# Performance work log

Hardware: AMD Instinct MI355X
Metric: run time of the kernel (lower is better)

Reference implementation:

```python
import jax, jax.numpy as jnp
import numpy as np


def _sparse_mask(T, S, W, G):
    """Replicates CustomSparseAttention._create_sparse_mask (bool [T, S])."""
    ii = np.arange(T)[:, None]
    jj = np.arange(S)[None, :]
    # local sliding window: cols in [i - W//2, i + W//2]
    m = (jj >= ii - W // 2) & (jj <= ii + W // 2)
    # overlapping block windows every (W - W//4) rows
    ov = W // 4
    for i in range(0, T, W - ov):
        m[i:i + W, max(0, i - ov):min(S, i + W + ov)] = True
    # strided global tokens
    if G > 0:
        stride = S // (G + 1)
        gi = np.linspace(stride, S - stride, G).astype(np.int64)  # torch .long() truncates
        m[:, gi] = True
    # diagonal +/- 1
    m |= np.abs(jj - ii) <= 1
    return jnp.asarray(m)


def setup_inputs() -> dict:
    key = jax.random.key(0)
    ks = jax.random.split(key, 8)
    B, T, S, E = 2, 2048, 2048, 512
    std = 0.02
    return {
        "query": jax.random.normal(ks[0], (B, T, E), jnp.float32),
        "key": jax.random.normal(ks[1], (B, S, E), jnp.float32),
        "value": jax.random.normal(ks[2], (B, S, E), jnp.float32),
        "Wq": jax.random.normal(ks[3], (E, E), jnp.float32) * std,
        "bq": jnp.zeros((E,), jnp.float32),
        "Wk": jax.random.normal(ks[4], (E, E), jnp.float32) * std,
        "bk": jnp.zeros((E,), jnp.float32),
        "Wv": jax.random.normal(ks[5], (E, E), jnp.float32) * std,
        "bv": jnp.zeros((E,), jnp.float32),
        "Wo": jax.random.normal(ks[6], (E, E), jnp.float32) * std,
        "bo": jnp.zeros((E,), jnp.float32),
        "temperature": jnp.ones((1,), jnp.float32) * 0.1,
        "local_window_size": 128,
        "num_global_tokens": 16,
    }


def reference(query, key, value, Wq, bq, Wk, bk, Wv, bv, Wo, bo,
              temperature, local_window_size, num_global_tokens):
    B, T, E = query.shape
    S = key.shape[1]
    H = 16
    hd = E // H
    scaling = float(hd) ** -0.5

    q = (query @ Wq.T + bq) * scaling          # [B, T, E]
    k = key @ Wk.T + bk                        # [B, S, E]
    v = value @ Wv.T + bv                      # [B, S, E]

    q = q.reshape(B, T, H, hd)
    k = k.reshape(B, S, H, hd)
    v = v.reshape(B, S, H, hd)

    # [B, H, T, S] dense scores, scaled by learned temperature
    attn = jnp.einsum('bthd,bshd->bhts', q, k) * temperature[0]

    mask = _sparse_mask(T, S, local_window_size, num_global_tokens)  # [T, S] bool
    attn = jnp.where(mask[None, None], attn, -jnp.inf)

    # (row-max subtraction in the original is the standard stable softmax)
    attn = jax.nn.softmax(attn, axis=-1)

    out = jnp.einsum('bhts,bshd->bthd', attn, v).reshape(B, T, E)
    out = out @ Wo.T + bo
    return out
```

## Files before the change

### kernel.cpp

```cpp
#include <hip/hip_runtime.h>

typedef _Float16 f16x8 __attribute__((ext_vector_type(8)));
typedef float f32x4 __attribute__((ext_vector_type(4)));

#define Tt 2048
#define Ee 512
#define Hh 16
#define HD 32
#define Bb 2
#define Mm (Bb*Tt)

__device__ __constant__ int GCOLS[16] = {120,240,361,481,602,722,843,963,
                                         1084,1204,1325,1445,1566,1686,1807,1928};

__device__ __forceinline__ int lo_of(int i) {
    int kmin = (i >= 32) ? ((i - 32) / 96) : 0;
    int lo = kmin * 96 - 32;
    return lo < 0 ? 0 : lo;
}
__device__ __forceinline__ int hi_of(int i) {
    int hi = (i / 96) * 96 + 160;
    return hi > Tt ? Tt : hi;
}

__device__ __forceinline__ f16x8 cvt8(float4 a, float4 b) {
    f16x8 r;
    r[0]=(_Float16)a.x; r[1]=(_Float16)a.y; r[2]=(_Float16)a.z; r[3]=(_Float16)a.w;
    r[4]=(_Float16)b.x; r[5]=(_Float16)b.y; r[6]=(_Float16)b.z; r[7]=(_Float16)b.w;
    return r;
}

__device__ __forceinline__ void async_copy16(const _Float16* g, _Float16* l) {
    __builtin_amdgcn_global_load_lds(
        (const __attribute__((address_space(1))) void*)g,
        (__attribute__((address_space(3))) void*)l, 16, 0, 0);
}

__global__ __launch_bounds__(256)
void cvt_kernel(const float* __restrict__ q, const float* __restrict__ k,
                const float* __restrict__ v,
                const float* __restrict__ wq, const float* __restrict__ wk,
                const float* __restrict__ wv, const float* __restrict__ wo,
                _Float16* __restrict__ dst)
{
    const int g8 = blockIdx.x * 256 + threadIdx.x;
    const float* src;
    if (g8 < 786432) {
        const int s = g8 >> 18;
        const float* xs = (s == 0) ? q : (s == 1) ? k : v;
        src = xs + (size_t)(g8 & 262143) * 8;
    } else {
        const int w8 = g8 - 786432;
        const int s = w8 >> 15;
        const float* ws = (s == 0) ? wq : (s == 1) ? wk : (s == 2) ? wv : wo;
        src = ws + (size_t)(w8 & 32767) * 8;
    }
    float4 a = ((const float4*)src)[0];
    float4 b = ((const float4*)src)[1];
    *(f16x8*)(dst + (size_t)g8 * 8) = cvt8(a, b);
}

__global__ __launch_bounds__(256)
void proj_kernel(const _Float16* __restrict__ xw,
                 const float* __restrict__ bq, const float* __restrict__ bk,
                 const float* __restrict__ bv, const float* __restrict__ temp,
                 _Float16* __restrict__ q_ws, _Float16* __restrict__ k_ws,
                 _Float16* __restrict__ v_ws)
{
    const int z = blockIdx.z;
    const _Float16* A = xw + (size_t)z * (Mm * Ee);
    const _Float16* W = xw + (size_t)3 * Mm * Ee + (size_t)z * (Ee * Ee);
    const float* bias = (z == 0) ? bq : (z == 1) ? bk : bv;

    const int m0 = blockIdx.x * 64;
    const int n0 = blockIdx.y * 128;

    __shared__ _Float16 Ash[64 * 64];
    __shared__ _Float16 Bsh[128 * 64];

    const int tid  = threadIdx.x;
    const int lane = tid & 63, wave = tid >> 6;
    const int quad = lane >> 4, l16 = lane & 15;
    const int wm = wave & 1, wn = wave >> 1;

    const int sl = lane >> 3;
    const int lcol = ((lane & 7) ^ sl) * 8;
    const _Float16* aSrc0 = A + (size_t)(m0 + wave*8       + sl) * Ee + lcol;
    const _Float16* aSrc1 = A + (size_t)(m0 + (4+wave)*8   + sl) * Ee + lcol;
    const _Float16* bSrc0 = W + (size_t)(n0 + wave*8       + sl) * Ee + lcol;
    const _Float16* bSrc1 = W + (size_t)(n0 + (4+wave)*8   + sl) * Ee + lcol;
    const _Float16* bSrc2 = W + (size_t)(n0 + (8+wave)*8   + sl) * Ee + lcol;
    const _Float16* bSrc3 = W + (size_t)(n0 + (12+wave)*8  + sl) * Ee + lcol;
    _Float16* aDst0 = Ash + wave*512;
    _Float16* aDst1 = Ash + (4+wave)*512;
    _Float16* bDst0 = Bsh + wave*512;
    _Float16* bDst1 = Bsh + (4+wave)*512;
    _Float16* bDst2 = Bsh + (8+wave)*512;
    _Float16* bDst3 = Bsh + (12+wave)*512;

    f32x4 acc[2][4] = {};

    for (int k0 = 0; k0 < Ee; k0 += 64) {
        __syncthreads();
        async_copy16(aSrc0 + k0, aDst0);
        async_copy16(aSrc1 + k0, aDst1);
        async_copy16(bSrc0 + k0, bDst0);
        async_copy16(bSrc1 + k0, bDst1);
        async_copy16(bSrc2 + k0, bDst2);
        async_copy16(bSrc3 + k0, bDst3);
        __syncthreads();

        #pragma unroll
        for (int kk = 0; kk < 2; kk++) {
            f16x8 af[2], bf[4];
            #pragma unroll
            for (int mt = 0; mt < 2; mt++) {
                const int row = wm*32 + mt*16 + l16;
                af[mt] = *(const f16x8*)&Ash[row*64 + (((kk*4+quad) ^ (row & 7)) * 8)];
            }
            #pragma unroll
            for (int nt = 0; nt < 4; nt++) {
                const int row = wn*64 + nt*16 + l16;
                bf[nt] = *(const f16x8*)&Bsh[row*64 + (((kk*4+quad) ^ (row & 7)) * 8)];
            }
            #pragma unroll
            for (int mt = 0; mt < 2; mt++)
                #pragma unroll
                for (int nt = 0; nt < 4; nt++)
                    acc[mt][nt] = __builtin_amdgcn_mfma_f32_16x16x32_f16(af[mt], bf[nt], acc[mt][nt], 0, 0, 0);
        }
    }

    const float scale = (z == 0) ? (0.17677669529663687f * temp[0]) : 1.0f;
    #pragma unroll
    for (int nt = 0; nt < 4; nt++) {
        const int n = n0 + wn * 64 + nt * 16 + l16;
        const float bn = bias[n];
        const int h = n >> 5, d = n & 31;
        #pragma unroll
        for (int mt = 0; mt < 2; mt++) {
            #pragma unroll
            for (int r = 0; r < 4; r++) {
                const int m = m0 + wm * 32 + mt * 16 + quad * 4 + r;
                const float val = (acc[mt][nt][r] + bn) * scale;
                const int bidx = m >> 11, t = m & (Tt - 1);
                if (z == 2) {
                    v_ws[((size_t)(bidx * Hh + h) * HD + d) * Tt + t] = (_Float16)val;
                } else {
                    _Float16* dst = (z == 0) ? q_ws : k_ws;
                    dst[((size_t)(bidx * Hh + h) * Tt + t) * HD + d] = (_Float16)val;
                }
            }
        }
    }
}

__global__ __launch_bounds__(256)
void attn_kernel(const _Float16* __restrict__ q_ws, const _Float16* __restrict__ k_ws,
                 const _Float16* __restrict__ v_ws, _Float16* __restrict__ o_ws)
{
    const int qb = blockIdx.x * 64;
    const int h  = blockIdx.y;
    const int b  = blockIdx.z;
    const int bh = b * Hh + h;

    const int tid  = threadIdx.x;
    const int lane = tid & 63, wave = tid >> 6;
    const int quad = lane >> 4, l16 = lane & 15;
    const int t0   = qb + wave * 16;

    __shared__ _Float16 P_lds[4][16*72];
    _Float16* myP = &P_lds[wave][0];

    const f16x8 qf = *(const f16x8*)(q_ws + ((size_t)bh*Tt + t0 + l16)*HD + quad*8);

    int lo[4], len[4];
    #pragma unroll
    for (int r = 0; r < 4; r++) {
        const int i = t0 + quad*4 + r;
        lo[r] = lo_of(i); len[r] = hi_of(i) - lo[r];
    }

    float lsum[4] = {0.f, 0.f, 0.f, 0.f};
    f32x4 accO[2] = {};
    const f32x4 zf = {0.f, 0.f, 0.f, 0.f};

    {
        const int gj = GCOLS[l16];
        const f16x8 kg = *(const f16x8*)(k_ws + ((size_t)bh*Tt + gj)*HD + quad*8);
        const f32x4 s = __builtin_amdgcn_mfma_f32_16x16x32_f16(qf, kg, zf, 0, 0, 0);
        #pragma unroll
        for (int r = 0; r < 4; r++) {
            const bool inside = (unsigned)(gj - lo[r]) < (unsigned)len[r];
            const float p = inside ? 0.f : __expf(s[r]);
            const _Float16 ph = (_Float16)p;
            lsum[r] += (float)ph;
            myP[(quad*4 + r)*72 + l16] = ph;
        }
        f16x8 pf;
        if (quad < 2) pf = *(const f16x8*)&myP[l16*72 + quad*8];
        else {
            #pragma unroll
            for (int j = 0; j < 8; j++) pf[j] = (_Float16)0.f;
        }
        int gck[8];
        #pragma unroll
        for (int j = 0; j < 8; j++) gck[j] = (quad < 2) ? GCOLS[quad*8 + j] : 0;
        #pragma unroll
        for (int dt = 0; dt < 2; dt++) {
            f16x8 vg;
            if (quad < 2) {
                const _Float16* vrow = v_ws + ((size_t)bh*HD + dt*16 + l16)*Tt;
                #pragma unroll
                for (int j = 0; j < 8; j++) vg[j] = vrow[gck[j]];
            } else {
                #pragma unroll
                for (int j = 0; j < 8; j++) vg[j] = (_Float16)0.f;
            }
            accO[dt] = __builtin_amdgcn_mfma_f32_16x16x32_f16(pf, vg, accO[dt], 0, 0, 0);
        }
    }

    const int cstart = lo_of(t0) & ~63;
    const int cend   = hi_of(t0 + 15);
    for (int j0 = cstart; j0 < cend; j0 += 64) {
        f16x8 kf[4]; f32x4 s[4];
        #pragma unroll
        for (int nt = 0; nt < 4; nt++)
            kf[nt] = *(const f16x8*)(k_ws + ((size_t)bh*Tt + j0 + nt*16 + l16)*HD + quad*8);
        #pragma unroll
        for (int nt = 0; nt < 4; nt++)
            s[nt] = __builtin_amdgcn_mfma_f32_16x16x32_f16(qf, kf[nt], zf, 0, 0, 0);
        #pragma unroll
        for (int nt = 0; nt < 4; nt++) {
            const int j = j0 + nt*16 + l16;
            #pragma unroll
            for (int r = 0; r < 4; r++) {
                const bool inside = (unsigned)(j - lo[r]) < (unsigned)len[r];
                const float p = inside ? __expf(s[nt][r]) : 0.f;
                const _Float16 ph = (_Float16)p;
                lsum[r] += (float)ph;
                myP[(quad*4 + r)*72 + nt*16 + l16] = ph;
            }
        }
        #pragma unroll
        for (int kt = 0; kt < 2; kt++) {
            const f16x8 pf = *(const f16x8*)&myP[l16*72 + kt*32 + quad*8];
            #pragma unroll
            for (int dt = 0; dt < 2; dt++) {
                const f16x8 vf = *(const f16x8*)(v_ws + ((size_t)bh*HD + dt*16 + l16)*Tt
                                                 + j0 + kt*32 + quad*8);
                accO[dt] = __builtin_amdgcn_mfma_f32_16x16x32_f16(pf, vf, accO[dt], 0, 0, 0);
            }
        }
    }

    #pragma unroll
    for (int r = 0; r < 4; r++) {
        float v = lsum[r];
        v += __shfl_xor(v, 1);
        v += __shfl_xor(v, 2);
        v += __shfl_xor(v, 4);
        v += __shfl_xor(v, 8);
        lsum[r] = 1.0f / v;
    }
    #pragma unroll
    for (int dt = 0; dt < 2; dt++) {
        #pragma unroll
        for (int r = 0; r < 4; r++) {
            const int t = t0 + quad*4 + r;
            const int d = dt*16 + l16;
            o_ws[((size_t)(b*Tt + t)*Hh + h)*HD + d] = (_Float16)(accO[dt][r] * lsum[r]);
        }
    }
}

__global__ __launch_bounds__(256)
void out_kernel(const _Float16* __restrict__ Aw, const _Float16* __restrict__ Wof,
                const float* __restrict__ bo, float* __restrict__ out)
{
    const int m0 = blockIdx.x * 64;
    const int n0 = blockIdx.y * 128;

    __shared__ _Float16 Ash[64 * 64];
    __shared__ _Float16 Bsh[128 * 64];

    const int tid  = threadIdx.x;
    const int lane = tid & 63, wave = tid >> 6;
    const int quad = lane >> 4, l16 = lane & 15;
    const int wm = wave & 1, wn = wave >> 1;

    const int sl = lane >> 3;
    const int lcol = ((lane & 7) ^ sl) * 8;
    const _Float16* aSrc0 = Aw  + (size_t)(m0 + wave*8      + sl) * Ee + lcol;
    const _Float16* aSrc1 = Aw  + (size_t)(m0 + (4+wave)*8  + sl) * Ee + lcol;
    const _Float16* bSrc0 = Wof + (size_t)(n0 + wave*8      + sl) * Ee + lcol;
    const _Float16* bSrc1 = Wof + (size_t)(n0 + (4+wave)*8  + sl) * Ee + lcol;
    const _Float16* bSrc2 = Wof + (size_t)(n0 + (8+wave)*8  + sl) * Ee + lcol;
    const _Float16* bSrc3 = Wof + (size_t)(n0 + (12+wave)*8 + sl) * Ee + lcol;
    _Float16* aDst0 = Ash + wave*512;
    _Float16* aDst1 = Ash + (4+wave)*512;
    _Float16* bDst0 = Bsh + wave*512;
    _Float16* bDst1 = Bsh + (4+wave)*512;
    _Float16* bDst2 = Bsh + (8+wave)*512;
    _Float16* bDst3 = Bsh + (12+wave)*512;

    f32x4 acc[2][4] = {};

    for (int k0 = 0; k0 < Ee; k0 += 64) {
        __syncthreads();
        async_copy16(aSrc0 + k0, aDst0);
        async_copy16(aSrc1 + k0, aDst1);
        async_copy16(bSrc0 + k0, bDst0);
        async_copy16(bSrc1 + k0, bDst1);
        async_copy16(bSrc2 + k0, bDst2);
        async_copy16(bSrc3 + k0, bDst3);
        __syncthreads();

        #pragma unroll
        for (int kk = 0; kk < 2; kk++) {
            f16x8 af[2], bf[4];
            #pragma unroll
            for (int mt = 0; mt < 2; mt++) {
                const int row = wm*32 + mt*16 + l16;
                af[mt] = *(const f16x8*)&Ash[row*64 + (((kk*4+quad) ^ (row & 7)) * 8)];
            }
            #pragma unroll
            for (int nt = 0; nt < 4; nt++) {
                const int row = wn*64 + nt*16 + l16;
                bf[nt] = *(const f16x8*)&Bsh[row*64 + (((kk*4+quad) ^ (row & 7)) * 8)];
            }
            #pragma unroll
            for (int mt = 0; mt < 2; mt++)
                #pragma unroll
                for (int nt = 0; nt < 4; nt++)
                    acc[mt][nt] = __builtin_amdgcn_mfma_f32_16x16x32_f16(af[mt], bf[nt], acc[mt][nt], 0, 0, 0);
        }
    }

    #pragma unroll
    for (int nt = 0; nt < 4; nt++) {
        const int n = n0 + wn * 64 + nt * 16 + l16;
        const float bn = bo[n];
        #pragma unroll
        for (int mt = 0; mt < 2; mt++) {
            #pragma unroll
            for (int r = 0; r < 4; r++) {
                const int m = m0 + wm * 32 + mt * 16 + quad * 4 + r;
                out[(size_t)m * Ee + n] = acc[mt][nt][r] + bn;
            }
        }
    }
}

extern "C" void kernel_launch(void* const* d_in, const int* in_sizes, int n_in,
                              void* d_out, int out_size, void* d_ws, size_t ws_size,
                              hipStream_t stream)
{
    const float* query = (const float*)d_in[0];
    const float* key_  = (const float*)d_in[1];
    const float* value = (const float*)d_in[2];
    const float* Wq    = (const float*)d_in[3];
    const float* bq    = (const float*)d_in[4];
    const float* Wk    = (const float*)d_in[5];
    const float* bk    = (const float*)d_in[6];
    const float* Wv    = (const float*)d_in[7];
    const float* bv    = (const float*)d_in[8];
    const float* Wo    = (const float*)d_in[9];
    const float* bo    = (const float*)d_in[10];
    const float* temp  = (const float*)d_in[11];

    _Float16* xw   = (_Float16*)d_ws;
    _Float16* q_ws = xw + 7340032;
    _Float16* k_ws = q_ws + (size_t)Mm * Ee;
    _Float16* v_ws = k_ws + (size_t)Mm * Ee;
    _Float16* o_ws = v_ws + (size_t)Mm * Ee;
    const _Float16* Wof = xw + (size_t)3 * Mm * Ee + (size_t)3 * Ee * Ee;
    float* out = (float*)d_out;

    cvt_kernel<<<3584, 256, 0, stream>>>(query, key_, value, Wq, Wk, Wv, Wo, xw);
    proj_kernel<<<dim3(64, 4, 3), 256, 0, stream>>>(xw, bq, bk, bv, temp,
                                                    q_ws, k_ws, v_ws);
    attn_kernel<<<dim3(32, 16, 2), 256, 0, stream>>>(q_ws, k_ws, v_ws, o_ws);
    out_kernel<<<dim3(64, 4), 256, 0, stream>>>(o_ws, Wof, bo, out);
}
```

Baseline: 142.1 us.

## Double-buffer LDS tiles in projection and output GEMM kernels

```diff
diff --git a/kernel.cpp b/kernel.cpp
--- a/kernel.cpp
+++ b/kernel.cpp
@@ -75,8 +75,8 @@
     const int m0 = blockIdx.x * 64;
     const int n0 = blockIdx.y * 128;
 
-    __shared__ _Float16 Ash[64 * 64];
-    __shared__ _Float16 Bsh[128 * 64];
+    __shared__ _Float16 Ash[2][64 * 64];
+    __shared__ _Float16 Bsh[2][128 * 64];
 
     const int tid  = threadIdx.x;
     const int lane = tid & 63, wave = tid >> 6;
@@ -91,24 +91,31 @@
     const _Float16* bSrc1 = W + (size_t)(n0 + (4+wave)*8   + sl) * Ee + lcol;
     const _Float16* bSrc2 = W + (size_t)(n0 + (8+wave)*8   + sl) * Ee + lcol;
     const _Float16* bSrc3 = W + (size_t)(n0 + (12+wave)*8  + sl) * Ee + lcol;
-    _Float16* aDst0 = Ash + wave*512;
-    _Float16* aDst1 = Ash + (4+wave)*512;
-    _Float16* bDst0 = Bsh + wave*512;
-    _Float16* bDst1 = Bsh + (4+wave)*512;
-    _Float16* bDst2 = Bsh + (8+wave)*512;
-    _Float16* bDst3 = Bsh + (12+wave)*512;
+
+#define PROJ_STAGE(BUF, K0)                                          \
+    do {                                                             \
+        async_copy16(aSrc0 + (K0), &Ash[BUF][ wave    * 512]);       \
+        async_copy16(aSrc1 + (K0), &Ash[BUF][( 4+wave)* 512]);       \
+        async_copy16(bSrc0 + (K0), &Bsh[BUF][ wave    * 512]);       \
+        async_copy16(bSrc1 + (K0), &Bsh[BUF][( 4+wave)* 512]);       \
+        async_copy16(bSrc2 + (K0), &Bsh[BUF][( 8+wave)* 512]);       \
+        async_copy16(bSrc3 + (K0), &Bsh[BUF][(12+wave)* 512]);       \
+    } while (0)
 
     f32x4 acc[2][4] = {};
 
-    for (int k0 = 0; k0 < Ee; k0 += 64) {
-        __syncthreads();
-        async_copy16(aSrc0 + k0, aDst0);
-        async_copy16(aSrc1 + k0, aDst1);
-        async_copy16(bSrc0 + k0, bDst0);
-        async_copy16(bSrc1 + k0, bDst1);
-        async_copy16(bSrc2 + k0, bDst2);
-        async_copy16(bSrc3 + k0, bDst3);
-        __syncthreads();
+    PROJ_STAGE(0, 0);
+
+    #pragma unroll
+    for (int it = 0; it < 8; ++it) {
+        const int cur = it & 1;
+        if (it < 7) {
+            PROJ_STAGE(cur ^ 1, (it + 1) * 64);
+            asm volatile("s_waitcnt vmcnt(6)" ::: "memory");
+        } else {
+            asm volatile("s_waitcnt vmcnt(0)" ::: "memory");
+        }
+        __builtin_amdgcn_s_barrier();
 
         #pragma unroll
         for (int kk = 0; kk < 2; kk++) {
@@ -116,12 +123,12 @@
             #pragma unroll
             for (int mt = 0; mt < 2; mt++) {
                 const int row = wm*32 + mt*16 + l16;
-                af[mt] = *(const f16x8*)&Ash[row*64 + (((kk*4+quad) ^ (row & 7)) * 8)];
+                af[mt] = *(const f16x8*)&Ash[cur][row*64 + (((kk*4+quad) ^ (row & 7)) * 8)];
             }
             #pragma unroll
             for (int nt = 0; nt < 4; nt++) {
                 const int row = wn*64 + nt*16 + l16;
-                bf[nt] = *(const f16x8*)&Bsh[row*64 + (((kk*4+quad) ^ (row & 7)) * 8)];
+                bf[nt] = *(const f16x8*)&Bsh[cur][row*64 + (((kk*4+quad) ^ (row & 7)) * 8)];
             }
             #pragma unroll
             for (int mt = 0; mt < 2; mt++)
@@ -129,7 +136,9 @@
                 for (int nt = 0; nt < 4; nt++)
                     acc[mt][nt] = __builtin_amdgcn_mfma_f32_16x16x32_f16(af[mt], bf[nt], acc[mt][nt], 0, 0, 0);
         }
-    }
+        __builtin_amdgcn_s_barrier();
+    }
+#undef PROJ_STAGE
 
     const float scale = (z == 0) ? (0.17677669529663687f * temp[0]) : 1.0f;
     #pragma unroll
@@ -282,8 +291,8 @@
     const int m0 = blockIdx.x * 64;
     const int n0 = blockIdx.y * 128;
 
-    __shared__ _Float16 Ash[64 * 64];
-    __shared__ _Float16 Bsh[128 * 64];
+    __shared__ _Float16 Ash[2][64 * 64];
+    __shared__ _Float16 Bsh[2][128 * 64];
 
     const int tid  = threadIdx.x;
     const int lane = tid & 63, wave = tid >> 6;
@@ -298,24 +307,31 @@
     const _Float16* bSrc1 = Wof + (size_t)(n0 + (4+wave)*8  + sl) * Ee + lcol;
     const _Float16* bSrc2 = Wof + (size_t)(n0 + (8+wave)*8  + sl) * Ee + lcol;
     const _Float16* bSrc3 = Wof + (size_t)(n0 + (12+wave)*8 + sl) * Ee + lcol;
-    _Float16* aDst0 = Ash + wave*512;
-    _Float16* aDst1 = Ash + (4+wave)*512;
-    _Float16* bDst0 = Bsh + wave*512;
-    _Float16* bDst1 = Bsh + (4+wave)*512;
-    _Float16* bDst2 = Bsh + (8+wave)*512;
-    _Float16* bDst3 = Bsh + (12+wave)*512;
+
+#define OUT_STAGE(BUF, K0)                                           \
+    do {                                                             \
+        async_copy16(aSrc0 + (K0), &Ash[BUF][ wave    * 512]);       \
+        async_copy16(aSrc1 + (K0), &Ash[BUF][( 4+wave)* 512]);       \
+        async_copy16(bSrc0 + (K0), &Bsh[BUF][ wave    * 512]);       \
+        async_copy16(bSrc1 + (K0), &Bsh[BUF][( 4+wave)* 512]);       \
+        async_copy16(bSrc2 + (K0), &Bsh[BUF][( 8+wave)* 512]);       \
+        async_copy16(bSrc3 + (K0), &Bsh[BUF][(12+wave)* 512]);       \
+    } while (0)
 
     f32x4 acc[2][4] = {};
 
-    for (int k0 = 0; k0 < Ee; k0 += 64) {
-        __syncthreads();
-        async_copy16(aSrc0 + k0, aDst0);
-        async_copy16(aSrc1 + k0, aDst1);
-        async_copy16(bSrc0 + k0, bDst0);
-        async_copy16(bSrc1 + k0, bDst1);
-        async_copy16(bSrc2 + k0, bDst2);
-        async_copy16(bSrc3 + k0, bDst3);
-        __syncthreads();
+    OUT_STAGE(0, 0);
+
+    #pragma unroll
+    for (int it = 0; it < 8; ++it) {
+        const int cur = it & 1;
+        if (it < 7) {
+            OUT_STAGE(cur ^ 1, (it + 1) * 64);
+            asm volatile("s_waitcnt vmcnt(6)" ::: "memory");
+        } else {
+            asm volatile("s_waitcnt vmcnt(0)" ::: "memory");
+        }
+        __builtin_amdgcn_s_barrier();
 
         #pragma unroll
         for (int kk = 0; kk < 2; kk++) {
@@ -323,12 +339,12 @@
             #pragma unroll
             for (int mt = 0; mt < 2; mt++) {
                 const int row = wm*32 + mt*16 + l16;
-                af[mt] = *(const f16x8*)&Ash[row*64 + (((kk*4+quad) ^ (row & 7)) * 8)];
+                af[mt] = *(const f16x8*)&Ash[cur][row*64 + (((kk*4+quad) ^ (row & 7)) * 8)];
             }
             #pragma unroll
             for (int nt = 0; nt < 4; nt++) {
                 const int row = wn*64 + nt*16 + l16;
-                bf[nt] = *(const f16x8*)&Bsh[row*64 + (((kk*4+quad) ^ (row & 7)) * 8)];
+                bf[nt] = *(const f16x8*)&Bsh[cur][row*64 + (((kk*4+quad) ^ (row & 7)) * 8)];
             }
             #pragma unroll
             for (int mt = 0; mt < 2; mt++)
@@ -336,7 +352,9 @@
                 for (int nt = 0; nt < 4; nt++)
                     acc[mt][nt] = __builtin_amdgcn_mfma_f32_16x16x32_f16(af[mt], bf[nt], acc[mt][nt], 0, 0, 0);
         }
-    }
+        __builtin_amdgcn_s_barrier();
+    }
+#undef OUT_STAGE
 
     #pragma unroll
     for (int nt = 0; nt < 4; nt++) {
```

Measured after the change: 141.8 us. No clear change (-0.3%).

## Fuse four kernel launches into one cooperative persistent kernel with grid syncs

Applied to the files above, without the earlier changes.

```diff
diff --git a/kernel.cpp b/kernel.cpp
--- a/kernel.cpp
+++ b/kernel.cpp
@@ -1,4 +1,7 @@
 #include <hip/hip_runtime.h>
+#include <hip/hip_cooperative_groups.h>
+
+namespace cg = cooperative_groups;
 
 typedef _Float16 f16x8 __attribute__((ext_vector_type(8)));
 typedef float f32x4 __attribute__((ext_vector_type(4)));
@@ -34,6 +37,304 @@
     __builtin_amdgcn_global_load_lds(
         (const __attribute__((address_space(1))) void*)g,
         (__attribute__((address_space(3))) void*)l, 16, 0, 0);
+}
+
+__global__ __launch_bounds__(256, 4)
+void fused_kernel(const float* __restrict__ query, const float* __restrict__ key_,
+                  const float* __restrict__ value,
+                  const float* __restrict__ Wq, const float* __restrict__ Wk,
+                  const float* __restrict__ Wv, const float* __restrict__ Wo,
+                  const float* __restrict__ bq, const float* __restrict__ bk,
+                  const float* __restrict__ bv, const float* __restrict__ bo,
+                  const float* __restrict__ temp,
+                  _Float16* __restrict__ ws, float* __restrict__ out)
+{
+    __shared__ _Float16 sh[12288];
+    _Float16* Ash = sh;
+    _Float16* Bsh = sh + 4096;
+
+    _Float16* xw   = ws;
+    _Float16* q_ws = ws + 7340032;
+    _Float16* k_ws = q_ws + (size_t)Mm * Ee;
+    _Float16* v_ws = k_ws + (size_t)Mm * Ee;
+    _Float16* o_ws = v_ws + (size_t)Mm * Ee;
+    const _Float16* Wof = ws + (size_t)3 * Mm * Ee + (size_t)3 * Ee * Ee;
+
+    const int tid  = threadIdx.x;
+    const int bid  = blockIdx.x;
+    const int lane = tid & 63, wave = tid >> 6;
+    const int quad = lane >> 4, l16 = lane & 15;
+
+    for (int u = bid * 256 + tid; u < 917504; u += 262144) {
+        const float* src;
+        if (u < 786432) {
+            const int s = u >> 18;
+            const float* xs = (s == 0) ? query : (s == 1) ? key_ : value;
+            src = xs + (size_t)(u & 262143) * 8;
+        } else {
+            const int w8 = u - 786432;
+            const int s = w8 >> 15;
+            const float* wsrc = (s == 0) ? Wq : (s == 1) ? Wk : (s == 2) ? Wv : Wo;
+            src = wsrc + (size_t)(w8 & 32767) * 8;
+        }
+        float4 a = ((const float4*)src)[0];
+        float4 b = ((const float4*)src)[1];
+        *(f16x8*)(xw + (size_t)u * 8) = cvt8(a, b);
+    }
+    cg::this_grid().sync();
+
+    if (bid < 768) {
+        const int z   = bid >> 8;
+        const int rem = bid & 255;
+        const int m0  = (rem >> 2) * 64;
+        const int n0  = (rem & 3) * 128;
+
+        const _Float16* A = xw + (size_t)z * (Mm * Ee);
+        const _Float16* W = xw + (size_t)3 * Mm * Ee + (size_t)z * (Ee * Ee);
+        const float* bias = (z == 0) ? bq : (z == 1) ? bk : bv;
+
+        const int wm = wave & 1, wn = wave >> 1;
+        const int sl = lane >> 3;
+        const int lcol = ((lane & 7) ^ sl) * 8;
+        const _Float16* aSrc0 = A + (size_t)(m0 + wave*8       + sl) * Ee + lcol;
+        const _Float16* aSrc1 = A + (size_t)(m0 + (4+wave)*8   + sl) * Ee + lcol;
+        const _Float16* bSrc0 = W + (size_t)(n0 + wave*8       + sl) * Ee + lcol;
+        const _Float16* bSrc1 = W + (size_t)(n0 + (4+wave)*8   + sl) * Ee + lcol;
+        const _Float16* bSrc2 = W + (size_t)(n0 + (8+wave)*8   + sl) * Ee + lcol;
+        const _Float16* bSrc3 = W + (size_t)(n0 + (12+wave)*8  + sl) * Ee + lcol;
+
+        f32x4 acc[2][4] = {};
+
+        for (int k0 = 0; k0 < Ee; k0 += 64) {
+            __syncthreads();
+            async_copy16(aSrc0 + k0, Ash + wave*512);
+            async_copy16(aSrc1 + k0, Ash + (4+wave)*512);
+            async_copy16(bSrc0 + k0, Bsh + wave*512);
+            async_copy16(bSrc1 + k0, Bsh + (4+wave)*512);
+            async_copy16(bSrc2 + k0, Bsh + (8+wave)*512);
+            async_copy16(bSrc3 + k0, Bsh + (12+wave)*512);
+            __syncthreads();
+
+            #pragma unroll
+            for (int kk = 0; kk < 2; kk++) {
+                f16x8 af[2], bf[4];
+                #pragma unroll
+                for (int mt = 0; mt < 2; mt++) {
+                    const int row = wm*32 + mt*16 + l16;
+                    af[mt] = *(const f16x8*)&Ash[row*64 + (((kk*4+quad) ^ (row & 7)) * 8)];
+                }
+                #pragma unroll
+                for (int nt = 0; nt < 4; nt++) {
+                    const int row = wn*64 + nt*16 + l16;
+                    bf[nt] = *(const f16x8*)&Bsh[row*64 + (((kk*4+quad) ^ (row & 7)) * 8)];
+                }
+                #pragma unroll
+                for (int mt = 0; mt < 2; mt++)
+                    #pragma unroll
+                    for (int nt = 0; nt < 4; nt++)
+                        acc[mt][nt] = __builtin_amdgcn_mfma_f32_16x16x32_f16(af[mt], bf[nt], acc[mt][nt], 0, 0, 0);
+            }
+        }
+
+        const float scale = (z == 0) ? (0.17677669529663687f * temp[0]) : 1.0f;
+        #pragma unroll
+        for (int nt = 0; nt < 4; nt++) {
+            const int n = n0 + wn * 64 + nt * 16 + l16;
+            const float bn = bias[n];
+            const int h = n >> 5, d = n & 31;
+            #pragma unroll
+            for (int mt = 0; mt < 2; mt++) {
+                #pragma unroll
+                for (int r = 0; r < 4; r++) {
+                    const int m = m0 + wm * 32 + mt * 16 + quad * 4 + r;
+                    const float val = (acc[mt][nt][r] + bn) * scale;
+                    const int bidx = m >> 11, t = m & (Tt - 1);
+                    if (z == 2) {
+                        v_ws[((size_t)(bidx * Hh + h) * HD + d) * Tt + t] = (_Float16)val;
+                    } else {
+                        _Float16* dst = (z == 0) ? q_ws : k_ws;
+                        dst[((size_t)(bidx * Hh + h) * Tt + t) * HD + d] = (_Float16)val;
+                    }
+                }
+            }
+        }
+    }
+    cg::this_grid().sync();
+
+    {
+        const int qb = (bid & 31) * 64;
+        const int h  = (bid >> 5) & 15;
+        const int b  = bid >> 9;
+        const int bh = b * Hh + h;
+        const int t0 = qb + wave * 16;
+
+        _Float16* myP = sh + wave * 1152;
+
+        const f16x8 qf = *(const f16x8*)(q_ws + ((size_t)bh*Tt + t0 + l16)*HD + quad*8);
+
+        int lo[4], len[4];
+        #pragma unroll
+        for (int r = 0; r < 4; r++) {
+            const int i = t0 + quad*4 + r;
+            lo[r] = lo_of(i); len[r] = hi_of(i) - lo[r];
+        }
+
+        float lsum[4] = {0.f, 0.f, 0.f, 0.f};
+        f32x4 accO[2] = {};
+        const f32x4 zf = {0.f, 0.f, 0.f, 0.f};
+
+        {
+            const int gj = GCOLS[l16];
+            const f16x8 kg = *(const f16x8*)(k_ws + ((size_t)bh*Tt + gj)*HD + quad*8);
+            const f32x4 s = __builtin_amdgcn_mfma_f32_16x16x32_f16(qf, kg, zf, 0, 0, 0);
+            #pragma unroll
+            for (int r = 0; r < 4; r++) {
+                const bool inside = (unsigned)(gj - lo[r]) < (unsigned)len[r];
+                const float p = inside ? 0.f : __expf(s[r]);
+                const _Float16 ph = (_Float16)p;
+                lsum[r] += (float)ph;
+                myP[(quad*4 + r)*72 + l16] = ph;
+            }
+            f16x8 pf;
+            if (quad < 2) pf = *(const f16x8*)&myP[l16*72 + quad*8];
+            else {
+                #pragma unroll
+                for (int j = 0; j < 8; j++) pf[j] = (_Float16)0.f;
+            }
+            int gck[8];
+            #pragma unroll
+            for (int j = 0; j < 8; j++) gck[j] = (quad < 2) ? GCOLS[quad*8 + j] : 0;
+            #pragma unroll
+            for (int dt = 0; dt < 2; dt++) {
+                f16x8 vg;
+                if (quad < 2) {
+                    const _Float16* vrow = v_ws + ((size_t)bh*HD + dt*16 + l16)*Tt;
+                    #pragma unroll
+                    for (int j = 0; j < 8; j++) vg[j] = vrow[gck[j]];
+                } else {
+                    #pragma unroll
+                    for (int j = 0; j < 8; j++) vg[j] = (_Float16)0.f;
+                }
+                accO[dt] = __builtin_amdgcn_mfma_f32_16x16x32_f16(pf, vg, accO[dt], 0, 0, 0);
+            }
+        }
+
+        const int cstart = lo_of(t0) & ~63;
+        const int cend   = hi_of(t0 + 15);
+        for (int j0 = cstart; j0 < cend; j0 += 64) {
+            f16x8 kf[4]; f32x4 s[4];
+            #pragma unroll
+            for (int nt = 0; nt < 4; nt++)
+                kf[nt] = *(const f16x8*)(k_ws + ((size_t)bh*Tt + j0 + nt*16 + l16)*HD + quad*8);
+            #pragma unroll
+            for (int nt = 0; nt < 4; nt++)
+                s[nt] = __builtin_amdgcn_mfma_f32_16x16x32_f16(qf, kf[nt], zf, 0, 0, 0);
+            #pragma unroll
+            for (int nt = 0; nt < 4; nt++) {
+                const int j = j0 + nt*16 + l16;
+                #pragma unroll
+                for (int r = 0; r < 4; r++) {
+                    const bool inside = (unsigned)(j - lo[r]) < (unsigned)len[r];
+                    const float p = inside ? __expf(s[nt][r]) : 0.f;
+                    const _Float16 ph = (_Float16)p;
+                    lsum[r] += (float)ph;
+                    myP[(quad*4 + r)*72 + nt*16 + l16] = ph;
+                }
+            }
+            #pragma unroll
+            for (int kt = 0; kt < 2; kt++) {
+                const f16x8 pf = *(const f16x8*)&myP[l16*72 + kt*32 + quad*8];
+                #pragma unroll
+                for (int dt = 0; dt < 2; dt++) {
+                    const f16x8 vf = *(const f16x8*)(v_ws + ((size_t)bh*HD + dt*16 + l16)*Tt
+                                                     + j0 + kt*32 + quad*8);
+                    accO[dt] = __builtin_amdgcn_mfma_f32_16x16x32_f16(pf, vf, accO[dt], 0, 0, 0);
+                }
+            }
+        }
+
+        #pragma unroll
+        for (int r = 0; r < 4; r++) {
+            float v = lsum[r];
+            v += __shfl_xor(v, 1);
+            v += __shfl_xor(v, 2);
+            v += __shfl_xor(v, 4);
+            v += __shfl_xor(v, 8);
+            lsum[r] = 1.0f / v;
+        }
+        #pragma unroll
+        for (int dt = 0; dt < 2; dt++) {
+            #pragma unroll
+            for (int r = 0; r < 4; r++) {
+                const int t = t0 + quad*4 + r;
+                const int d = dt*16 + l16;
+                o_ws[((size_t)(b*Tt + t)*Hh + h)*HD + d] = (_Float16)(accO[dt][r] * lsum[r]);
+            }
+        }
+    }
+    cg::this_grid().sync();
+
+    if (bid < 256) {
+        const int m0 = (bid >> 2) * 64;
+        const int n0 = (bid & 3) * 128;
+
+        const int wm = wave & 1, wn = wave >> 1;
+        const int sl = lane >> 3;
+        const int lcol = ((lane & 7) ^ sl) * 8;
+        const _Float16* aSrc0 = o_ws + (size_t)(m0 + wave*8      + sl) * Ee + lcol;
+        const _Float16* aSrc1 = o_ws + (size_t)(m0 + (4+wave)*8  + sl) * Ee + lcol;
+        const _Float16* bSrc0 = Wof  + (size_t)(n0 + wave*8      + sl) * Ee + lcol;
+        const _Float16* bSrc1 = Wof  + (size_t)(n0 + (4+wave)*8  + sl) * Ee + lcol;
+        const _Float16* bSrc2 = Wof  + (size_t)(n0 + (8+wave)*8  + sl) * Ee + lcol;
+        const _Float16* bSrc3 = Wof  + (size_t)(n0 + (12+wave)*8 + sl) * Ee + lcol;
+
+        f32x4 acc[2][4] = {};
+
+        for (int k0 = 0; k0 < Ee; k0 += 64) {
+            __syncthreads();
+            async_copy16(aSrc0 + k0, Ash + wave*512);
+            async_copy16(aSrc1 + k0, Ash + (4+wave)*512);
+            async_copy16(bSrc0 + k0, Bsh + wave*512);
+            async_copy16(bSrc1 + k0, Bsh + (4+wave)*512);
+            async_copy16(bSrc2 + k0, Bsh + (8+wave)*512);
+            async_copy16(bSrc3 + k0, Bsh + (12+wave)*512);
+            __syncthreads();
+
+            #pragma unroll
+            for (int kk = 0; kk < 2; kk++) {
+                f16x8 af[2], bf[4];
+                #pragma unroll
+                for (int mt = 0; mt < 2; mt++) {
+                    const int row = wm*32 + mt*16 + l16;
+                    af[mt] = *(const f16x8*)&Ash[row*64 + (((kk*4+quad) ^ (row & 7)) * 8)];
+                }
+                #pragma unroll
+                for (int nt = 0; nt < 4; nt++) {
+                    const int row = wn*64 + nt*16 + l16;
+                    bf[nt] = *(const f16x8*)&Bsh[row*64 + (((kk*4+quad) ^ (row & 7)) * 8)];
+                }
+                #pragma unroll
+                for (int mt = 0; mt < 2; mt++)
+                    #pragma unroll
+                    for (int nt = 0; nt < 4; nt++)
+                        acc[mt][nt] = __builtin_amdgcn_mfma_f32_16x16x32_f16(af[mt], bf[nt], acc[mt][nt], 0, 0, 0);
+            }
+        }
+
+        #pragma unroll
+        for (int nt = 0; nt < 4; nt++) {
+            const int n = n0 + wn * 64 + nt * 16 + l16;
+            const float bn = bo[n];
+            #pragma unroll
+            for (int mt = 0; mt < 2; mt++) {
+                #pragma unroll
+                for (int r = 0; r < 4; r++) {
+                    const int m = m0 + wm * 32 + mt * 16 + quad * 4 + r;
+                    out[(size_t)m * Ee + n] = acc[mt][nt][r] + bn;
+                }
+            }
+        }
+    }
 }
 
 __global__ __launch_bounds__(256)
@@ -91,23 +392,17 @@
     const _Float16* bSrc1 = W + (size_t)(n0 + (4+wave)*8   + sl) * Ee + lcol;
     const _Float16* bSrc2 = W + (size_t)(n0 + (8+wave)*8   + sl) * Ee + lcol;
     const _Float16* bSrc3 = W + (size_t)(n0 + (12+wave)*8  + sl) * Ee + lcol;
-    _Float16* aDst0 = Ash + wave*512;
-    _Float16* aDst1 = Ash + (4+wave)*512;
-    _Float16* bDst0 = Bsh + wave*512;
-    _Float16* bDst1 = Bsh + (4+wave)*512;
-    _Float16* bDst2 = Bsh + (8+wave)*512;
-    _Float16* bDst3 = Bsh + (12+wave)*512;
 
     f32x4 acc[2][4] = {};
 
     for (int k0 = 0; k0 < Ee; k0 += 64) {
         __syncthreads();
-        async_copy16(aSrc0 + k0, aDst0);
-        async_copy16(aSrc1 + k0, aDst1);
-        async_copy16(bSrc0 + k0, bDst0);
-        async_copy16(bSrc1 + k0, bDst1);
-        async_copy16(bSrc2 + k0, bDst2);
-        async_copy16(bSrc3 + k0, bDst3);
+        async_copy16(aSrc0 + k0, Ash + wave*512);
+        async_copy16(aSrc1 + k0, Ash + (4+wave)*512);
+        async_copy16(bSrc0 + k0, Bsh + wave*512);
+        async_copy16(bSrc1 + k0, Bsh + (4+wave)*512);
+        async_copy16(bSrc2 + k0, Bsh + (8+wave)*512);
+        async_copy16(bSrc3 + k0, Bsh + (12+wave)*512);
         __syncthreads();
 
         #pragma unroll
@@ -298,23 +593,17 @@
     const _Float16* bSrc1 = Wof + (size_t)(n0 + (4+wave)*8  + sl) * Ee + lcol;
     const _Float16* bSrc2 = Wof + (size_t)(n0 + (8+wave)*8  + sl) * Ee + lcol;
     const _Float16* bSrc3 = Wof + (size_t)(n0 + (12+wave)*8 + sl) * Ee + lcol;
-    _Float16* aDst0 = Ash + wave*512;
-    _Float16* aDst1 = Ash + (4+wave)*512;
-    _Float16* bDst0 = Bsh + wave*512;
-    _Float16* bDst1 = Bsh + (4+wave)*512;
-    _Float16* bDst2 = Bsh + (8+wave)*512;
-    _Float16* bDst3 = Bsh + (12+wave)*512;
 
     f32x4 acc[2][4] = {};
 
     for (int k0 = 0; k0 < Ee; k0 += 64) {
         __syncthreads();
-        async_copy16(aSrc0 + k0, aDst0);
-        async_copy16(aSrc1 + k0, aDst1);
-        async_copy16(bSrc0 + k0, bDst0);
-        async_copy16(bSrc1 + k0, bDst1);
-        async_copy16(bSrc2 + k0, bDst2);
-        async_copy16(bSrc3 + k0, bDst3);
+        async_copy16(aSrc0 + k0, Ash + wave*512);
+        async_copy16(aSrc1 + k0, Ash + (4+wave)*512);
+        async_copy16(bSrc0 + k0, Bsh + wave*512);
+        async_copy16(bSrc1 + k0, Bsh + (4+wave)*512);
+        async_copy16(bSrc2 + k0, Bsh + (8+wave)*512);
+        async_copy16(bSrc3 + k0, Bsh + (12+wave)*512);
         __syncthreads();
 
         #pragma unroll
@@ -370,17 +659,30 @@
     const float* bo    = (const float*)d_in[10];
     const float* temp  = (const float*)d_in[11];
 
-    _Float16* xw   = (_Float16*)d_ws;
-    _Float16* q_ws = xw + 7340032;
-    _Float16* k_ws = q_ws + (size_t)Mm * Ee;
-    _Float16* v_ws = k_ws + (size_t)Mm * Ee;
-    _Float16* o_ws = v_ws + (size_t)Mm * Ee;
-    const _Float16* Wof = xw + (size_t)3 * Mm * Ee + (size_t)3 * Ee * Ee;
-    float* out = (float*)d_out;
-
-    cvt_kernel<<<3584, 256, 0, stream>>>(query, key_, value, Wq, Wk, Wv, Wo, xw);
-    proj_kernel<<<dim3(64, 4, 3), 256, 0, stream>>>(xw, bq, bk, bv, temp,
-                                                    q_ws, k_ws, v_ws);
-    attn_kernel<<<dim3(32, 16, 2), 256, 0, stream>>>(q_ws, k_ws, v_ws, o_ws);
-    out_kernel<<<dim3(64, 4), 256, 0, stream>>>(o_ws, Wof, bo, out);
-}
+    _Float16* ws  = (_Float16*)d_ws;
+    float*    out = (float*)d_out;
+
+    void* kargs[] = {
+        (void*)&query, (void*)&key_, (void*)&value,
+        (void*)&Wq, (void*)&Wk, (void*)&Wv, (void*)&Wo,
+        (void*)&bq, (void*)&bk, (void*)&bv, (void*)&bo, (void*)&temp,
+        (void*)&ws, (void*)&out
+    };
+    hipError_t err = hipLaunchCooperativeKernel(
+        (const void*)fused_kernel, dim3(1024), dim3(256), kargs, 0, stream);
+
+    if (err != hipSuccess) {
+        _Float16* xw   = ws;
+        _Float16* q_ws = xw + 7340032;
+        _Float16* k_ws = q_ws + (size_t)Mm * Ee;
+        _Float16* v_ws = k_ws + (size_t)Mm * Ee;
+        _Float16* o_ws = v_ws + (size_t)Mm * Ee;
+        const _Float16* Wof = xw + (size_t)3 * Mm * Ee + (size_t)3 * Ee * Ee;
+
+        cvt_kernel<<<3584, 256, 0, stream>>>(query, key_, value, Wq, Wk, Wv, Wo, xw);
+        proj_kernel<<<dim3(64, 4, 3), 256, 0, stream>>>(xw, bq, bk, bv, temp,
+                                                        q_ws, k_ws, v_ws);
+        attn_kernel<<<dim3(32, 16, 2), 256, 0, stream>>>(q_ws, k_ws, v_ws, o_ws);
+        out_kernel<<<dim3(64, 4), 256, 0, stream>>>(o_ws, Wof, bo, out);
+    }
+}
```

Measured after the change: 553.8 us. 290% more time.

## Fuse fp32-to-fp16 conversion into projection GEMM with register prefetch

Applied to the files above, without the earlier changes.

```diff
diff --git a/kernel.cpp b/kernel.cpp
--- a/kernel.cpp
+++ b/kernel.cpp
@@ -37,40 +37,30 @@
 }
 
 __global__ __launch_bounds__(256)
-void cvt_kernel(const float* __restrict__ q, const float* __restrict__ k,
-                const float* __restrict__ v,
-                const float* __restrict__ wq, const float* __restrict__ wk,
-                const float* __restrict__ wv, const float* __restrict__ wo,
-                _Float16* __restrict__ dst)
-{
-    const int g8 = blockIdx.x * 256 + threadIdx.x;
-    const float* src;
-    if (g8 < 786432) {
-        const int s = g8 >> 18;
-        const float* xs = (s == 0) ? q : (s == 1) ? k : v;
-        src = xs + (size_t)(g8 & 262143) * 8;
-    } else {
-        const int w8 = g8 - 786432;
-        const int s = w8 >> 15;
-        const float* ws = (s == 0) ? wq : (s == 1) ? wk : (s == 2) ? wv : wo;
-        src = ws + (size_t)(w8 & 32767) * 8;
-    }
-    float4 a = ((const float4*)src)[0];
-    float4 b = ((const float4*)src)[1];
-    *(f16x8*)(dst + (size_t)g8 * 8) = cvt8(a, b);
-}
-
-__global__ __launch_bounds__(256)
-void proj_kernel(const _Float16* __restrict__ xw,
+void proj_kernel(const float* __restrict__ qx, const float* __restrict__ kx,
+                 const float* __restrict__ vx,
+                 const float* __restrict__ Wq, const float* __restrict__ Wk,
+                 const float* __restrict__ Wv, const float* __restrict__ Wo,
                  const float* __restrict__ bq, const float* __restrict__ bk,
                  const float* __restrict__ bv, const float* __restrict__ temp,
                  _Float16* __restrict__ q_ws, _Float16* __restrict__ k_ws,
-                 _Float16* __restrict__ v_ws)
+                 _Float16* __restrict__ v_ws, _Float16* __restrict__ wof)
 {
     const int z = blockIdx.z;
-    const _Float16* A = xw + (size_t)z * (Mm * Ee);
-    const _Float16* W = xw + (size_t)3 * Mm * Ee + (size_t)z * (Ee * Ee);
+    const float* A = (z == 0) ? qx : (z == 1) ? kx : vx;
+    const float* W = (z == 0) ? Wq : (z == 1) ? Wk : Wv;
     const float* bias = (z == 0) ? bq : (z == 1) ? bk : bv;
+
+    {
+        const int fb = blockIdx.x + 64 * blockIdx.y + 256 * blockIdx.z;
+        if (fb < 128) {
+            const int g8 = fb * 256 + threadIdx.x;
+            const float* src = Wo + (size_t)g8 * 8;
+            float4 a = ((const float4*)src)[0];
+            float4 b = ((const float4*)src)[1];
+            *(f16x8*)(wof + (size_t)g8 * 8) = cvt8(a, b);
+        }
+    }
 
     const int m0 = blockIdx.x * 64;
     const int n0 = blockIdx.y * 128;
@@ -85,29 +75,59 @@
 
     const int sl = lane >> 3;
     const int lcol = ((lane & 7) ^ sl) * 8;
-    const _Float16* aSrc0 = A + (size_t)(m0 + wave*8       + sl) * Ee + lcol;
-    const _Float16* aSrc1 = A + (size_t)(m0 + (4+wave)*8   + sl) * Ee + lcol;
-    const _Float16* bSrc0 = W + (size_t)(n0 + wave*8       + sl) * Ee + lcol;
-    const _Float16* bSrc1 = W + (size_t)(n0 + (4+wave)*8   + sl) * Ee + lcol;
-    const _Float16* bSrc2 = W + (size_t)(n0 + (8+wave)*8   + sl) * Ee + lcol;
-    const _Float16* bSrc3 = W + (size_t)(n0 + (12+wave)*8  + sl) * Ee + lcol;
-    _Float16* aDst0 = Ash + wave*512;
-    _Float16* aDst1 = Ash + (4+wave)*512;
-    _Float16* bDst0 = Bsh + wave*512;
-    _Float16* bDst1 = Bsh + (4+wave)*512;
-    _Float16* bDst2 = Bsh + (8+wave)*512;
-    _Float16* bDst3 = Bsh + (12+wave)*512;
+    const float* aS[2] = {
+        A + (size_t)(m0 + wave*8      + sl) * Ee + lcol,
+        A + (size_t)(m0 + (4+wave)*8  + sl) * Ee + lcol };
+    const float* bS[4] = {
+        W + (size_t)(n0 + wave*8      + sl) * Ee + lcol,
+        W + (size_t)(n0 + (4+wave)*8  + sl) * Ee + lcol,
+        W + (size_t)(n0 + (8+wave)*8  + sl) * Ee + lcol,
+        W + (size_t)(n0 + (12+wave)*8 + sl) * Ee + lcol };
+    _Float16* aD[2] = { Ash + wave*512 + lane*8, Ash + (4+wave)*512 + lane*8 };
+    _Float16* bD[4] = { Bsh + wave*512 + lane*8, Bsh + (4+wave)*512 + lane*8,
+                        Bsh + (8+wave)*512 + lane*8, Bsh + (12+wave)*512 + lane*8 };
+
+    float4 pa[2][2][2];
+    float4 pb[2][4][2];
+
+    #pragma unroll
+    for (int u = 0; u < 2; ++u) {
+        pa[0][u][0] = ((const float4*)(aS[u]))[0];
+        pa[0][u][1] = ((const float4*)(aS[u]))[1];
+    }
+    #pragma unroll
+    for (int u = 0; u < 4; ++u) {
+        pb[0][u][0] = ((const float4*)(bS[u]))[0];
+        pb[0][u][1] = ((const float4*)(bS[u]))[1];
+    }
 
     f32x4 acc[2][4] = {};
 
-    for (int k0 = 0; k0 < Ee; k0 += 64) {
+    #pragma unroll
+    for (int it = 0; it < 8; ++it) {
+        const int cur = it & 1, nxt = cur ^ 1;
+
         __syncthreads();
-        async_copy16(aSrc0 + k0, aDst0);
-        async_copy16(aSrc1 + k0, aDst1);
-        async_copy16(bSrc0 + k0, bDst0);
-        async_copy16(bSrc1 + k0, bDst1);
-        async_copy16(bSrc2 + k0, bDst2);
-        async_copy16(bSrc3 + k0, bDst3);
+        #pragma unroll
+        for (int u = 0; u < 2; ++u)
+            *(f16x8*)aD[u] = cvt8(pa[cur][u][0], pa[cur][u][1]);
+        #pragma unroll
+        for (int u = 0; u < 4; ++u)
+            *(f16x8*)bD[u] = cvt8(pb[cur][u][0], pb[cur][u][1]);
+
+        if (it < 7) {
+            const int k0 = (it + 1) * 64;
+            #pragma unroll
+            for (int u = 0; u < 2; ++u) {
+                pa[nxt][u][0] = ((const float4*)(aS[u] + k0))[0];
+                pa[nxt][u][1] = ((const float4*)(aS[u] + k0))[1];
+            }
+            #pragma unroll
+            for (int u = 0; u < 4; ++u) {
+                pb[nxt][u][0] = ((const float4*)(bS[u] + k0))[0];
+                pb[nxt][u][1] = ((const float4*)(bS[u] + k0))[1];
+            }
+        }
         __syncthreads();
 
         #pragma unroll
@@ -298,23 +318,17 @@
     const _Float16* bSrc1 = Wof + (size_t)(n0 + (4+wave)*8  + sl) * Ee + lcol;
     const _Float16* bSrc2 = Wof + (size_t)(n0 + (8+wave)*8  + sl) * Ee + lcol;
     const _Float16* bSrc3 = Wof + (size_t)(n0 + (12+wave)*8 + sl) * Ee + lcol;
-    _Float16* aDst0 = Ash + wave*512;
-    _Float16* aDst1 = Ash + (4+wave)*512;
-    _Float16* bDst0 = Bsh + wave*512;
-    _Float16* bDst1 = Bsh + (4+wave)*512;
-    _Float16* bDst2 = Bsh + (8+wave)*512;
-    _Float16* bDst3 = Bsh + (12+wave)*512;
 
     f32x4 acc[2][4] = {};
 
     for (int k0 = 0; k0 < Ee; k0 += 64) {
         __syncthreads();
-        async_copy16(aSrc0 + k0, aDst0);
-        async_copy16(aSrc1 + k0, aDst1);
-        async_copy16(bSrc0 + k0, bDst0);
-        async_copy16(bSrc1 + k0, bDst1);
-        async_copy16(bSrc2 + k0, bDst2);
-        async_copy16(bSrc3 + k0, bDst3);
+        async_copy16(aSrc0 + k0, Ash + wave*512);
+        async_copy16(aSrc1 + k0, Ash + (4+wave)*512);
+        async_copy16(bSrc0 + k0, Bsh + wave*512);
+        async_copy16(bSrc1 + k0, Bsh + (4+wave)*512);
+        async_copy16(bSrc2 + k0, Bsh + (8+wave)*512);
+        async_copy16(bSrc3 + k0, Bsh + (12+wave)*512);
         __syncthreads();
 
         #pragma unroll
@@ -375,12 +389,13 @@
     _Float16* k_ws = q_ws + (size_t)Mm * Ee;
     _Float16* v_ws = k_ws + (size_t)Mm * Ee;
     _Float16* o_ws = v_ws + (size_t)Mm * Ee;
-    const _Float16* Wof = xw + (size_t)3 * Mm * Ee + (size_t)3 * Ee * Ee;
+    _Float16* wof  = xw + (size_t)3 * Mm * Ee + (size_t)3 * Ee * Ee;
     float* out = (float*)d_out;
 
-    cvt_kernel<<<3584, 256, 0, stream>>>(query, key_, value, Wq, Wk, Wv, Wo, xw);
-    proj_kernel<<<dim3(64, 4, 3), 256, 0, stream>>>(xw, bq, bk, bv, temp,
-                                                    q_ws, k_ws, v_ws);
+    proj_kernel<<<dim3(64, 4, 3), 256, 0, stream>>>(query, key_, value,
+                                                    Wq, Wk, Wv, Wo,
+                                                    bq, bk, bv, temp,
+                                                    q_ws, k_ws, v_ws, wof);
     attn_kernel<<<dim3(32, 16, 2), 256, 0, stream>>>(q_ws, k_ws, v_ws, o_ws);
-    out_kernel<<<dim3(64, 4), 256, 0, stream>>>(o_ws, Wof, bo, out);
-}
+    out_kernel<<<dim3(64, 4), 256, 0, stream>>>(o_ws, wof, bo, out);
+}
```

New measurement: 144.3 us. About the same (+1.5%).
